# Performance work log

Measured on AMD Instinct MI355X. Metric: run time of the kernel, lower is better.

## Reference

```python
import jax, jax.numpy as jnp
import numpy as np

B, S, D, H, F, V, K = 8, 1024, 1024, 16, 4096, 8192, 64
HD = D // H
ALPHA = 0.1


def layernorm(x, g, b, eps=1e-5):
    mu = jnp.mean(x, axis=-1, keepdims=True)
    var = jnp.var(x, axis=-1, keepdims=True)
    return (x - mu) * jax.lax.rsqrt(var + eps) * g + b


def setup_inputs() -> dict:
    key = jax.random.key(0)
    ks = jax.random.split(key, 16)
    s = lambda fan: 1.0 / np.sqrt(fan)
    inp = {
        "x": jax.random.normal(ks[0], (B, S, D), jnp.float32),
        "token_ids": jax.random.randint(ks[1], (B, S), 0, V),
        "pmi": jax.random.normal(ks[2], (V, V), jnp.float32) * 0.1,
        "Wq": jax.random.normal(ks[3], (D, D), jnp.float32) * s(D),
        "bq": jnp.zeros((D,), jnp.float32),
        "Wk": jax.random.normal(ks[4], (D, D), jnp.float32) * s(D),
        "bk": jnp.zeros((D,), jnp.float32),
        "Wv": jax.random.normal(ks[5], (D, D), jnp.float32) * s(D),
        "bv": jnp.zeros((D,), jnp.float32),
        "Wo": jax.random.normal(ks[6], (D, D), jnp.float32) * s(D),
        "bo": jnp.zeros((D,), jnp.float32),
        "W1": jax.random.normal(ks[7], (D, F), jnp.float32) * s(D),
        "b1": jnp.zeros((F,), jnp.float32),
        "W2": jax.random.normal(ks[8], (F, D), jnp.float32) * s(F),
        "b2": jnp.zeros((D,), jnp.float32),
        "g1": jnp.ones((D,), jnp.float32),
        "be1": jnp.zeros((D,), jnp.float32),
        "g2": jnp.ones((D,), jnp.float32),
        "be2": jnp.zeros((D,), jnp.float32),
    }
    return inp


def reference(x, token_ids, pmi, Wq, bq, Wk, bk, Wv, bv, Wo, bo,
              W1, b1, W2, b2, g1, be1, g2, be2):
    # --- SparseStatAttention: QK^T + alpha*PMI bias, top-k mask, softmax ---
    q = (x @ Wq + bq).reshape(B, S, H, HD)
    k = (x @ Wk + bk).reshape(B, S, H, HD)
    v = (x @ Wv + bv).reshape(B, S, H, HD)
    scores = jnp.einsum("bihd,bjhd->bhij", q, k) / np.sqrt(HD)  # [B,H,S,S]
    bias = pmi[token_ids[:, :, None], token_ids[:, None, :]]     # [B,S,S]
    scores = scores + ALPHA * bias[:, None, :, :]
    # top-k sparsification per query row (threshold at k-th largest value)
    kth = jax.lax.top_k(scores, K)[0][..., -1:]
    scores = jnp.where(scores >= kth, scores, -jnp.inf)
    w = jax.nn.softmax(scores, axis=-1)
    attn = jnp.einsum("bhij,bjhd->bihd", w, v).reshape(B, S, D)
    attn = attn @ Wo + bo
    # --- residual + norm1 (dropout is identity in eval) ---
    h = layernorm(x + attn, g1, be1)
    # --- GELU FFN (torch nn.GELU default = exact erf) ---
    ff = jax.nn.gelu(h @ W1 + b1, approximate=False) @ W2 + b2
    return layernorm(h + ff, g2, be2)
```

## Files before the change

### kernel.cpp

```cpp
#include <hip/hip_runtime.h>
#include <cstdint>
#include <cstddef>

#define B_   8
#define S_   1024
#define D_   1024
#define H_   16
#define HD_  64
#define F_   4096
#define V_   8192
#define KTOP 64

typedef unsigned short ushort_t;
typedef __attribute__((ext_vector_type(8))) short short8;
typedef __attribute__((ext_vector_type(8))) _Float16 half8;
typedef __attribute__((ext_vector_type(4))) float floatx4;
typedef __attribute__((ext_vector_type(4))) unsigned int uintx4;
typedef __attribute__((ext_vector_type(4))) float floatv4;
typedef __attribute__((ext_vector_type(4))) unsigned short ushortx4;
typedef __attribute__((ext_vector_type(8))) unsigned short ushortx8;

__device__ __forceinline__ ushort_t f2bf(float f) {
    unsigned int u = __builtin_bit_cast(unsigned int, f);
    u += 0x7fffu + ((u >> 16) & 1u);
    return (ushort_t)(u >> 16);
}
__device__ __forceinline__ float bf2f(ushort_t u) {
    unsigned int x = ((unsigned int)u) << 16;
    return __builtin_bit_cast(float, x);
}
__device__ __forceinline__ ushort_t f2h(float f) {
    _Float16 h = (_Float16)f;
    return __builtin_bit_cast(ushort_t, h);
}
__device__ __forceinline__ float h2f(ushort_t u) {
    return (float)__builtin_bit_cast(_Float16, u);
}

__device__ __forceinline__ void gload_lds16(const ushort_t* g, ushort_t* lds_base) {
    __builtin_amdgcn_global_load_lds(
        (const __attribute__((address_space(1))) unsigned int*)g,
        (__attribute__((address_space(3))) unsigned int*)lds_base,
        16, 0, 0);
}

__global__ __launch_bounds__(256) void cast_x_kernel(const float* __restrict__ x,
                                                     ushort_t* __restrict__ xb) {
    int gid = blockIdx.x * 256 + threadIdx.x;
    floatv4 v = ((const floatv4*)x)[gid];
    ushortx4 o;
    o[0] = f2bf(v[0]); o[1] = f2bf(v[1]); o[2] = f2bf(v[2]); o[3] = f2bf(v[3]);
    ((ushortx4*)xb)[gid] = o;
}

__global__ void transpose_cast_kernel(const float* __restrict__ W, ushort_t* __restrict__ WT,
                                      int K, int N, float scale) {
    __shared__ float tile[32][33];
    int n0 = blockIdx.x * 32, k0 = blockIdx.y * 32;
    #pragma unroll
    for (int i = threadIdx.y; i < 32; i += 8)
        tile[i][threadIdx.x] = W[(size_t)(k0 + i) * N + n0 + threadIdx.x];
    __syncthreads();
    #pragma unroll
    for (int i = threadIdx.y; i < 32; i += 8)
        WT[(size_t)(n0 + i) * K + k0 + threadIdx.x] = f2bf(tile[threadIdx.x][i] * scale);
}

__global__ __launch_bounds__(256) void pack_bias3_kernel(const float* __restrict__ bq,
                                                         const float* __restrict__ bk,
                                                         const float* __restrict__ bv,
                                                         float* __restrict__ o) {
    int i = blockIdx.x * 256 + threadIdx.x;
    float v = (i < 1024) ? bq[i] * 0.125f : (i < 2048) ? bk[i - 1024] : bv[i - 2048];
    o[i] = v;
}

__global__ __launch_bounds__(256) void bias_gather_kernel(const int* __restrict__ tok,
                                                          const float* __restrict__ pmi,
                                                          ushort_t* __restrict__ biasb) {
    int b = blockIdx.x >> 10;
    int i = blockIdx.x & (S_ - 1);
    int ti = tok[b * S_ + i];
    const float* prow = pmi + (size_t)ti * V_;
    #pragma unroll
    for (int it = 0; it < 4; it++) {
        int j = threadIdx.x + it * 256;
        int tj = tok[b * S_ + j];
        biasb[(size_t)blockIdx.x * S_ + j] = f2h(0.1f * prow[tj]);
    }
}

__global__ __launch_bounds__(256) void transpose_v_kernel(const ushort_t* __restrict__ v,
                                                          ushort_t* __restrict__ vT) {
    __shared__ ushort_t t[64 * 72];
    int bh = blockIdx.x >> 4;
    int s0 = (blockIdx.x & 15) * 64;
    #pragma unroll
    for (int it = 0; it < 2; it++) {
        int idx = threadIdx.x + it * 256;
        int sl = idx >> 3, dg = (idx & 7) * 8;
        *(uintx4*)&t[sl * 72 + dg] = *(const uintx4*)&v[((size_t)bh * S_ + s0 + sl) * HD_ + dg];
    }
    __syncthreads();
    #pragma unroll
    for (int it = 0; it < 2; it++) {
        int idx = threadIdx.x + it * 256;
        int dl = idx >> 3, sg = (idx & 7) * 8;
        ushortx8 o;
        #pragma unroll
        for (int i = 0; i < 8; i++) o[i] = f2h(bf2f(t[(sg + i) * 72 + dl]));
        *(ushortx8*)&vT[((size_t)bh * HD_ + dl) * S_ + s0 + sg] = o;
    }
}

__global__ __launch_bounds__(256) void gemm_bt(const ushort_t* __restrict__ A,
                                               const ushort_t* __restrict__ BT,
                                               const float* __restrict__ bias,
                                               ushort_t* __restrict__ C,
                                               int M, int N, int K, int ep) {
    __shared__ ushort_t As[128 * 32];
    __shared__ ushort_t Bs[128 * 32];

    const int tid = threadIdx.x;
    const int wid = tid >> 6, lane = tid & 63;
    const int quad = lane >> 4, r = lane & 15;
    const int wr = wid >> 1, wc = wid & 1;
    const int m0 = blockIdx.y * 128, n0 = blockIdx.x * 128;

    floatx4 acc[4][4];
    #pragma unroll
    for (int a = 0; a < 4; a++)
        #pragma unroll
        for (int b = 0; b < 4; b++) acc[a][b] = (floatx4){0.f, 0.f, 0.f, 0.f};

    const int srow = wid * 16 + (lane >> 2);
    const int scol = (lane & 3) * 8;
    const ushort_t* Ag0 = A + (size_t)(m0 + srow) * K + scol;
    const ushort_t* Ag1 = A + (size_t)(m0 + 64 + srow) * K + scol;
    const ushort_t* Bg0 = BT + (size_t)(n0 + srow) * K + scol;
    const ushort_t* Bg1 = BT + (size_t)(n0 + 64 + srow) * K + scol;
    ushort_t* Asd0 = As + (wid * 16) * 32;
    ushort_t* Asd1 = As + (64 + wid * 16) * 32;
    ushort_t* Bsd0 = Bs + (wid * 16) * 32;
    ushort_t* Bsd1 = Bs + (64 + wid * 16) * 32;

    for (int k0 = 0; k0 < K; k0 += 32) {
        __syncthreads();
        gload_lds16(Ag0 + k0, Asd0);
        gload_lds16(Ag1 + k0, Asd1);
        gload_lds16(Bg0 + k0, Bsd0);
        gload_lds16(Bg1 + k0, Bsd1);
        __syncthreads();

        short8 af[4], bf[4];
        #pragma unroll
        for (int t = 0; t < 4; t++)
            af[t] = *(const short8*)&As[(wr * 64 + t * 16 + r) * 32 + quad * 8];
        #pragma unroll
        for (int t = 0; t < 4; t++)
            bf[t] = *(const short8*)&Bs[(wc * 64 + t * 16 + r) * 32 + quad * 8];
        #pragma unroll
        for (int tm = 0; tm < 4; tm++)
            #pragma unroll
            for (int tn = 0; tn < 4; tn++)
                acc[tm][tn] = __builtin_amdgcn_mfma_f32_16x16x32_bf16(af[tm], bf[tn], acc[tm][tn], 0, 0, 0);
    }

    #pragma unroll
    for (int tm = 0; tm < 4; tm++) {
        #pragma unroll
        for (int tn = 0; tn < 4; tn++) {
            const int n = n0 + wc * 64 + tn * 16 + r;
            const float bv = bias[n];
            #pragma unroll
            for (int i2 = 0; i2 < 4; i2++) {
                const int m = m0 + wr * 64 + tm * 16 + quad * 4 + i2;
                float v = acc[tm][tn][i2] + bv;
                if (ep == 1) v = 0.5f * v * (1.0f + erff(v * 0.70710678118654752f));
                size_t idx;
                if (ep == 2) {
                    int tensor = n >> 10, nn = n & 1023;
                    idx = (size_t)tensor * (B_ * S_ * D_)
                        + (((size_t)(m >> 10) * H_ + (nn >> 6)) * S_ + (m & (S_ - 1))) * HD_ + (nn & (HD_ - 1));
                } else {
                    idx = (size_t)m * N + n;
                }
                C[idx] = f2bf(v);
            }
        }
    }
}

__global__ __launch_bounds__(256) void attn_kernel(const ushort_t* __restrict__ q,
                                                   const ushort_t* __restrict__ k,
                                                   const ushort_t* __restrict__ vT,
                                                   const ushort_t* __restrict__ biasb,
                                                   ushort_t* __restrict__ attnb) {
    extern __shared__ char smem[];
    ushort_t* Sm = (ushort_t*)smem;
    _Float16* Smh = (_Float16*)smem;

    const int bid = blockIdx.x;
    const int b = bid >> 10;
    const int h = (bid >> 6) & (H_ - 1);
    const int i0 = (bid & 63) * 16;
    const int tid = threadIdx.x;
    const int wid = tid >> 6, lane = tid & 63;
    const int quad = lane >> 4, r = lane & 15;

    const size_t bh = (size_t)b * H_ + h;
    const ushort_t* qbase = q + bh * S_ * HD_;
    const ushort_t* kbase = k + bh * S_ * HD_;
    const ushort_t* vbase = vT + bh * HD_ * S_;
    const ushort_t* bsrc = biasb + ((size_t)b * S_ + i0) * S_;

    #pragma unroll
    for (int c8 = 0; c8 < 8; c8++) {
        int c = wid * 8 + c8;
        int row = c >> 1, half = c & 1;
        int xr = row & 7;
        gload_lds16(bsrc + (size_t)row * S_ + half * 512 + (lane ^ xr) * 8,
                    Sm + row * 1024 + half * 512);
    }
    short8 aq0 = *(const short8*)&qbase[(size_t)(i0 + r) * HD_ + quad * 8];
    short8 aq1 = *(const short8*)&qbase[(size_t)(i0 + r) * HD_ + 32 + quad * 8];
    __syncthreads();

    #pragma unroll 4
    for (int t = 0; t < 16; t++) {
        int jt = (t * 4 + wid) * 16;
        int cb = (jt + r) >> 3;
        int co = r & 7;
        floatx4 acc;
        int la[4];
        #pragma unroll
        for (int i2 = 0; i2 < 4; i2++) {
            int row = quad * 4 + i2;
            la[i2] = row * 1024 + ((cb ^ (row & 7)) << 3) + co;
            acc[i2] = (float)Smh[la[i2]];
        }
        const ushort_t* kp = kbase + (size_t)(jt + r) * HD_ + quad * 8;
        short8 b0 = *(const short8*)kp;
        short8 b1 = *(const short8*)(kp + 32);
        acc = __builtin_amdgcn_mfma_f32_16x16x32_bf16(aq0, b0, acc, 0, 0, 0);
        acc = __builtin_amdgcn_mfma_f32_16x16x32_bf16(aq1, b1, acc, 0, 0, 0);
        #pragma unroll
        for (int i2 = 0; i2 < 4; i2++)
            Smh[la[i2]] = (_Float16)acc[i2];
    }
    __syncthreads();

    for (int rr = 0; rr < 4; rr++) {
        int row = wid * 4 + rr;
        ushort_t* Srow = Sm + row * 1024;
        ushortx8 u0 = *(const ushortx8*)&Srow[lane * 8];
        ushortx8 u1 = *(const ushortx8*)&Srow[(64 + lane) * 8];
        unsigned int kk[16];
        unsigned int lmax = 0u;
        #pragma unroll
        for (int t = 0; t < 8; t++) {
            unsigned int ua = u0[t];
            kk[t] = ua ^ ((ua & 0x8000u) ? 0xFFFFu : 0x8000u);
            lmax = kk[t] > lmax ? kk[t] : lmax;
            unsigned int ub = u1[t];
            kk[8 + t] = ub ^ ((ub & 0x8000u) ? 0xFFFFu : 0x8000u);
            lmax = kk[8 + t] > lmax ? kk[8 + t] : lmax;
        }
        unsigned int M = lmax, T0 = lmax;
        #pragma unroll
        for (int off = 32; off; off >>= 1) {
            unsigned int om = (unsigned int)__shfl_xor((int)M, off);
            unsigned int ot = (unsigned int)__shfl_xor((int)T0, off);
            M = om > M ? om : M;
            T0 = ot < T0 ? ot : T0;
        }
        float mx = h2f((ushort_t)((M & 0x8000u) ? (M ^ 0x8000u) : (~M & 0xFFFFu)));
        unsigned int T;
        int hb;
        unsigned int diff = T0 ^ M;
        if (diff == 0u) { T = M; hb = -1; }
        else { hb = 31 - __builtin_clz(diff); T = M & ~((2u << hb) - 1u); }
        for (int bit = hb; bit >= 0; bit--) {
            unsigned int trial = T | (1u << bit);
            int c = 0;
            #pragma unroll
            for (int t = 0; t < 16; t++)
                c += __popcll(__ballot(kk[t] >= trial));
            if (c >= KTOP) {
                T = trial;
                if (c == KTOP) break;
            }
        }
        float ev[16]; float sum = 0.f;
        #pragma unroll
        for (int t = 0; t < 8; t++) {
            float sa = h2f((ushort_t)u0[t]);
            float ea = (kk[t] >= T) ? __expf(sa - mx) : 0.f;
            ev[t] = ea; sum += ea;
            float sb = h2f((ushort_t)u1[t]);
            float eb = (kk[8 + t] >= T) ? __expf(sb - mx) : 0.f;
            ev[8 + t] = eb; sum += eb;
        }
        #pragma unroll
        for (int off = 32; off; off >>= 1) sum += __shfl_xor(sum, off);
        float inv = 1.f / sum;
        ushortx8 w0, w1;
        #pragma unroll
        for (int t = 0; t < 8; t++) {
            w0[t] = f2h(ev[t] * inv);
            w1[t] = f2h(ev[8 + t] * inv);
        }
        *(ushortx8*)&Srow[lane * 8] = w0;
        *(ushortx8*)&Srow[(64 + lane) * 8] = w1;
    }
    __syncthreads();

    floatx4 o0 = (floatx4){0.f, 0.f, 0.f, 0.f};
    floatx4 o1 = (floatx4){0.f, 0.f, 0.f, 0.f};
    const _Float16* Srowp = Smh + (size_t)r * 1024;
    const int xr = r & 7;
    const ushort_t* vrow = vbase + (size_t)(wid * 16 + r) * S_;
    #pragma unroll 4
    for (int ks2 = 0; ks2 < 16; ks2++) {
        int ks = ks2 * 2;
        half8 wa0 = *(const half8*)&Srowp[((ks * 4 + quad) ^ xr) << 3];
        half8 wa1 = *(const half8*)&Srowp[(((ks + 1) * 4 + quad) ^ xr) << 3];
        half8 vb0 = *(const half8*)&vrow[ks * 32 + quad * 8];
        half8 vb1 = *(const half8*)&vrow[(ks + 1) * 32 + quad * 8];
        o0 = __builtin_amdgcn_mfma_f32_16x16x32_f16(wa0, vb0, o0, 0, 0, 0);
        o1 = __builtin_amdgcn_mfma_f32_16x16x32_f16(wa1, vb1, o1, 0, 0, 0);
    }
    floatx4 oacc = o0 + o1;
    #pragma unroll
    for (int i2 = 0; i2 < 4; i2++) {
        int row = quad * 4 + i2;
        attnb[((size_t)b * S_ + i0 + row) * D_ + h * HD_ + wid * 16 + r] = f2bf(oacc[i2]);
    }
}

__global__ __launch_bounds__(256) void ln1_kernel(const float* __restrict__ x,
                                                  const ushort_t* __restrict__ t,
                                                  const float* __restrict__ g,
                                                  const float* __restrict__ be,
                                                  ushort_t* __restrict__ hb) {
    int row = blockIdx.x, tid = threadIdx.x;
    const float* xr = x + (size_t)row * D_;
    const ushort_t* tr = t + (size_t)row * D_;
    float v[4]; float s = 0.f, s2 = 0.f;
    #pragma unroll
    for (int it = 0; it < 4; it++) {
        int j = tid + it * 256;
        v[it] = xr[j] + bf2f(tr[j]);
        s += v[it]; s2 += v[it] * v[it];
    }
    #pragma unroll
    for (int off = 32; off; off >>= 1) { s += __shfl_xor(s, off); s2 += __shfl_xor(s2, off); }
    __shared__ float rs[4], rq[4];
    if ((tid & 63) == 0) { rs[tid >> 6] = s; rq[tid >> 6] = s2; }
    __syncthreads();
    s = rs[0] + rs[1] + rs[2] + rs[3];
    s2 = rq[0] + rq[1] + rq[2] + rq[3];
    float mu = s * (1.f / D_);
    float var = s2 * (1.f / D_) - mu * mu;
    float rstd = rsqrtf(var + 1e-5f);
    #pragma unroll
    for (int it = 0; it < 4; it++) {
        int j = tid + it * 256;
        hb[(size_t)row * D_ + j] = f2bf((v[it] - mu) * rstd * g[j] + be[j]);
    }
}

__global__ __launch_bounds__(256) void ln2_kernel(const ushort_t* __restrict__ hbuf,
                                                  const ushort_t* __restrict__ t,
                                                  const float* __restrict__ g,
                                                  const float* __restrict__ be,
                                                  float* __restrict__ out) {
    int row = blockIdx.x, tid = threadIdx.x;
    const ushort_t* hr = hbuf + (size_t)row * D_;
    const ushort_t* tr = t + (size_t)row * D_;
    float v[4]; float s = 0.f, s2 = 0.f;
    #pragma unroll
    for (int it = 0; it < 4; it++) {
        int j = tid + it * 256;
        v[it] = bf2f(hr[j]) + bf2f(tr[j]);
        s += v[it]; s2 += v[it] * v[it];
    }
    #pragma unroll
    for (int off = 32; off; off >>= 1) { s += __shfl_xor(s, off); s2 += __shfl_xor(s2, off); }
    __shared__ float rs[4], rq[4];
    if ((tid & 63) == 0) { rs[tid >> 6] = s; rq[tid >> 6] = s2; }
    __syncthreads();
    s = rs[0] + rs[1] + rs[2] + rs[3];
    s2 = rq[0] + rq[1] + rq[2] + rq[3];
    float mu = s * (1.f / D_);
    float var = s2 * (1.f / D_) - mu * mu;
    float rstd = rsqrtf(var + 1e-5f);
    #pragma unroll
    for (int it = 0; it < 4; it++) {
        int j = tid + it * 256;
        out[(size_t)row * D_ + j] = (v[it] - mu) * rstd * g[j] + be[j];
    }
}

extern "C" void kernel_launch(void* const* d_in, const int* in_sizes, int n_in,
                              void* d_out, int out_size, void* d_ws, size_t ws_size,
                              hipStream_t stream) {
    (void)in_sizes; (void)n_in; (void)out_size; (void)ws_size;
    const float* x   = (const float*)d_in[0];
    const int*   tok = (const int*)d_in[1];
    const float* pmi = (const float*)d_in[2];
    const float* Wq  = (const float*)d_in[3];
    const float* bq  = (const float*)d_in[4];
    const float* Wk  = (const float*)d_in[5];
    const float* bk  = (const float*)d_in[6];
    const float* Wv  = (const float*)d_in[7];
    const float* bv  = (const float*)d_in[8];
    const float* Wo  = (const float*)d_in[9];
    const float* bo  = (const float*)d_in[10];
    const float* W1  = (const float*)d_in[11];
    const float* b1  = (const float*)d_in[12];
    const float* W2  = (const float*)d_in[13];
    const float* b2  = (const float*)d_in[14];
    const float* g1  = (const float*)d_in[15];
    const float* be1 = (const float*)d_in[16];
    const float* g2  = (const float*)d_in[17];
    const float* be2 = (const float*)d_in[18];
    float* out = (float*)d_out;

    char* ws = (char*)d_ws;
    size_t off = 0;
    auto alloc = [&](size_t bytes) { char* p = ws + off; off += (bytes + 255) & ~(size_t)255; return p; };
    const size_t BSD = (size_t)B_ * S_ * D_;
    ushort_t* xb     = (ushort_t*)alloc(BSD * 2);
    ushort_t* WqkvT  = (ushort_t*)alloc((size_t)3 * D_ * D_ * 2);
    ushort_t* WoT    = (ushort_t*)alloc((size_t)D_ * D_ * 2);
    ushort_t* W1T    = (ushort_t*)alloc((size_t)D_ * F_ * 2);
    ushort_t* W2T    = (ushort_t*)alloc((size_t)F_ * D_ * 2);
    float*    bqkv   = (float*)alloc(3072 * 4);
    ushort_t* qkvb   = (ushort_t*)alloc(3 * BSD * 2);
    ushort_t* vT     = (ushort_t*)alloc(BSD * 2);
    ushort_t* biasb  = (ushort_t*)alloc((size_t)B_ * S_ * S_ * 2);
    ushort_t* extra  = (ushort_t*)alloc(BSD * 2);
    (void)extra;
    ushort_t* qb    = qkvb;
    ushort_t* kb    = qkvb + BSD;
    ushort_t* vb    = qkvb + 2 * BSD;
    ushort_t* attnb = xb;
    ushort_t* tbuf  = qb;
    ushort_t* hb    = kb;
    ushort_t* ffb   = vb;

    const size_t attn_lds = 16 * 1024 * 2;

    cast_x_kernel<<<8192, 256, 0, stream>>>(x, xb);
    transpose_cast_kernel<<<dim3(32, 32), dim3(32, 8), 0, stream>>>(Wq, WqkvT, D_, D_, 0.125f);
    transpose_cast_kernel<<<dim3(32, 32), dim3(32, 8), 0, stream>>>(Wk, WqkvT + (size_t)D_ * D_, D_, D_, 1.0f);
    transpose_cast_kernel<<<dim3(32, 32), dim3(32, 8), 0, stream>>>(Wv, WqkvT + (size_t)2 * D_ * D_, D_, D_, 1.0f);
    transpose_cast_kernel<<<dim3(32, 32), dim3(32, 8), 0, stream>>>(Wo, WoT, D_, D_, 1.0f);
    transpose_cast_kernel<<<dim3(128, 32), dim3(32, 8), 0, stream>>>(W1, W1T, D_, F_, 1.0f);
    transpose_cast_kernel<<<dim3(32, 128), dim3(32, 8), 0, stream>>>(W2, W2T, F_, D_, 1.0f);
    pack_bias3_kernel<<<12, 256, 0, stream>>>(bq, bk, bv, bqkv);
    bias_gather_kernel<<<B_ * S_, 256, 0, stream>>>(tok, pmi, biasb);

    gemm_bt<<<dim3(24, 64), 256, 0, stream>>>(xb, WqkvT, bqkv, qkvb, B_ * S_, 3 * D_, D_, 2);
    transpose_v_kernel<<<B_ * H_ * (S_ / 64), 256, 0, stream>>>(vb, vT);

    attn_kernel<<<B_ * H_ * (S_ / 16), 256, attn_lds, stream>>>(qb, kb, vT, biasb, attnb);

    gemm_bt<<<dim3(8, 64), 256, 0, stream>>>(attnb, WoT, bo, tbuf, B_ * S_, D_, D_, 0);
    ln1_kernel<<<B_ * S_, 256, 0, stream>>>(x, tbuf, g1, be1, hb);
    gemm_bt<<<dim3(32, 64), 256, 0, stream>>>(hb, W1T, b1, ffb, B_ * S_, F_, D_, 1);
    gemm_bt<<<dim3(8, 64), 256, 0, stream>>>(ffb, W2T, b2, tbuf, B_ * S_, D_, F_, 0);
    ln2_kernel<<<B_ * S_, 256, 0, stream>>>(hb, tbuf, g2, be2, out);
}
```

Measured before the change: 1.148 ms.

## Double-buffer GEMM LDS tiles and transpose QK MFMA for vectorized score access

The generic bf16 GEMM now uses two LDS buffers per operand. Each iteration prefetches the next K-slice while the MFMAs run on the current one, so only one barrier is needed per iteration instead of two. In the attention score pass, the MFMA operands are swapped so each lane owns four consecutive key columns of one query row. This allows a single 8-byte LDS load and store of the PMI bias and scores in place of four scalar accesses. LDS usage in the GEMM doubles, which may reduce occupancy, and the swizzle indexing changes, which risks layout mistakes.

```diff
diff --git a/kernel.cpp b/kernel.cpp
--- a/kernel.cpp
+++ b/kernel.cpp
@@ -118,8 +118,8 @@
                                                const float* __restrict__ bias,
                                                ushort_t* __restrict__ C,
                                                int M, int N, int K, int ep) {
-    __shared__ ushort_t As[128 * 32];
-    __shared__ ushort_t Bs[128 * 32];
+    __shared__ ushort_t As[2][128 * 32];
+    __shared__ ushort_t Bs[2][128 * 32];
 
     const int tid = threadIdx.x;
     const int wid = tid >> 6, lane = tid & 63;
@@ -139,31 +139,38 @@
     const ushort_t* Ag1 = A + (size_t)(m0 + 64 + srow) * K + scol;
     const ushort_t* Bg0 = BT + (size_t)(n0 + srow) * K + scol;
     const ushort_t* Bg1 = BT + (size_t)(n0 + 64 + srow) * K + scol;
-    ushort_t* Asd0 = As + (wid * 16) * 32;
-    ushort_t* Asd1 = As + (64 + wid * 16) * 32;
-    ushort_t* Bsd0 = Bs + (wid * 16) * 32;
-    ushort_t* Bsd1 = Bs + (64 + wid * 16) * 32;
-
+    const int d0 = (wid * 16) * 32;
+    const int d1 = (64 + wid * 16) * 32;
+
+    gload_lds16(Ag0, &As[0][d0]);
+    gload_lds16(Ag1, &As[0][d1]);
+    gload_lds16(Bg0, &Bs[0][d0]);
+    gload_lds16(Bg1, &Bs[0][d1]);
+    __syncthreads();
+
+    int cur = 0;
     for (int k0 = 0; k0 < K; k0 += 32) {
-        __syncthreads();
-        gload_lds16(Ag0 + k0, Asd0);
-        gload_lds16(Ag1 + k0, Asd1);
-        gload_lds16(Bg0 + k0, Bsd0);
-        gload_lds16(Bg1 + k0, Bsd1);
-        __syncthreads();
-
+        const int nxt = cur ^ 1;
+        if (k0 + 32 < K) {
+            gload_lds16(Ag0 + k0 + 32, &As[nxt][d0]);
+            gload_lds16(Ag1 + k0 + 32, &As[nxt][d1]);
+            gload_lds16(Bg0 + k0 + 32, &Bs[nxt][d0]);
+            gload_lds16(Bg1 + k0 + 32, &Bs[nxt][d1]);
+        }
         short8 af[4], bf[4];
         #pragma unroll
         for (int t = 0; t < 4; t++)
-            af[t] = *(const short8*)&As[(wr * 64 + t * 16 + r) * 32 + quad * 8];
+            af[t] = *(const short8*)&As[cur][(wr * 64 + t * 16 + r) * 32 + quad * 8];
         #pragma unroll
         for (int t = 0; t < 4; t++)
-            bf[t] = *(const short8*)&Bs[(wc * 64 + t * 16 + r) * 32 + quad * 8];
+            bf[t] = *(const short8*)&Bs[cur][(wc * 64 + t * 16 + r) * 32 + quad * 8];
         #pragma unroll
         for (int tm = 0; tm < 4; tm++)
             #pragma unroll
             for (int tn = 0; tn < 4; tn++)
                 acc[tm][tn] = __builtin_amdgcn_mfma_f32_16x16x32_bf16(af[tm], bf[tn], acc[tm][tn], 0, 0, 0);
+        __syncthreads();
+        cur = nxt;
     }
 
     #pragma unroll
@@ -226,27 +233,23 @@
     short8 aq1 = *(const short8*)&qbase[(size_t)(i0 + r) * HD_ + 32 + quad * 8];
     __syncthreads();
 
+    const int low3 = 2 * wid + (quad >> 1);
+    const int labase = r * 1024 + ((low3 ^ (r & 7)) << 3) + (quad & 1) * 4;
+    const ushort_t* kpl = kbase + (size_t)(wid * 16 + r) * HD_ + quad * 8;
     #pragma unroll 4
     for (int t = 0; t < 16; t++) {
-        int jt = (t * 4 + wid) * 16;
-        int cb = (jt + r) >> 3;
-        int co = r & 7;
+        const int la = labase + t * 64;
+        ushortx4 bi = *(const ushortx4*)&Sm[la];
         floatx4 acc;
-        int la[4];
-        #pragma unroll
-        for (int i2 = 0; i2 < 4; i2++) {
-            int row = quad * 4 + i2;
-            la[i2] = row * 1024 + ((cb ^ (row & 7)) << 3) + co;
-            acc[i2] = (float)Smh[la[i2]];
-        }
-        const ushort_t* kp = kbase + (size_t)(jt + r) * HD_ + quad * 8;
+        acc[0] = h2f(bi[0]); acc[1] = h2f(bi[1]); acc[2] = h2f(bi[2]); acc[3] = h2f(bi[3]);
+        const ushort_t* kp = kpl + (size_t)t * 64 * HD_;
         short8 b0 = *(const short8*)kp;
         short8 b1 = *(const short8*)(kp + 32);
-        acc = __builtin_amdgcn_mfma_f32_16x16x32_bf16(aq0, b0, acc, 0, 0, 0);
-        acc = __builtin_amdgcn_mfma_f32_16x16x32_bf16(aq1, b1, acc, 0, 0, 0);
-        #pragma unroll
-        for (int i2 = 0; i2 < 4; i2++)
-            Smh[la[i2]] = (_Float16)acc[i2];
+        acc = __builtin_amdgcn_mfma_f32_16x16x32_bf16(b0, aq0, acc, 0, 0, 0);
+        acc = __builtin_amdgcn_mfma_f32_16x16x32_bf16(b1, aq1, acc, 0, 0, 0);
+        ushortx4 so;
+        so[0] = f2h(acc[0]); so[1] = f2h(acc[1]); so[2] = f2h(acc[2]); so[3] = f2h(acc[3]);
+        *(ushortx4*)&Sm[la] = so;
     }
     __syncthreads();
 
```

New measurement: 1.100 ms. -4.2%, faster.
